# Kernel optimization log

Measured on AMD Instinct MI355X. Metric: run time of the kernel, lower is better.

## Reference

```python
import jax, jax.numpy as jnp
import numpy as np

B, C_ENC, H, W = 8, 512, 96, 96
N_SAMP = 64            # num_samples in forward
N_NODES = 2 * N_SAMP   # 64 pos + 64 neg per image
D = 256                # node feature dim after head_in_ln
N_HEADS = 8
DH = D // N_HEADS
SINKHORN_ITERS = 10


def _ln(x):
    # LayerNorm(elementwise_affine=False)
    m = x.mean(-1, keepdims=True)
    v = x.var(-1, keepdims=True)
    return (x - m) / jnp.sqrt(v + 1e-5)


def setup_inputs() -> dict:
    key = jax.random.key(0)
    ks = jax.random.split(key, 12)
    std = 0.01  # matches nn.init.normal_(std=0.01) in _init_weights
    inp = {
        "feat_s": jax.random.normal(ks[0], (B, C_ENC, H, W), jnp.float32),
        "score_s": jax.random.normal(ks[1], (B, 1, H, W), jnp.float32),
        "feat_t": jax.random.normal(ks[2], (B, C_ENC, H, W), jnp.float32),
        "score_t": jax.random.normal(ks[3], (B, 1, H, W), jnp.float32),
        "head_W1": std * jax.random.normal(ks[4], (C_ENC, D), jnp.float32),
        "head_b1": jnp.zeros((D,), jnp.float32),
        "head_W2": std * jax.random.normal(ks[5], (D, D), jnp.float32),
        "head_b2": jnp.zeros((D,), jnp.float32),
        "intra_W": jax.random.normal(ks[6], (4, D, D), jnp.float32) / jnp.sqrt(jnp.float32(D)),
        "intra_b": jnp.zeros((4, D), jnp.float32),
        "cross_W": jax.random.normal(ks[7], (4, D, D), jnp.float32) / jnp.sqrt(jnp.float32(D)),
        "cross_b": jnp.zeros((4, D), jnp.float32),
        "cls_W1": std * jax.random.normal(ks[8], (D, 128), jnp.float32),
        "cls_b1": jnp.zeros((128,), jnp.float32),
        "cls_W2": std * jax.random.normal(ks[9], (128, 1), jnp.float32),
        "cls_b2": jnp.zeros((1,), jnp.float32),
        "aff_A": jax.random.normal(ks[10], (D, D), jnp.float32) / jnp.sqrt(jnp.float32(D)),
    }
    return inp


def _sample_points(feat, score):
    # torch version: boolean-mask nonzero + random gather of 64 pos / 64 neg spatial
    # locations per image. JIT-friendly deterministic equivalent: top-64 highest
    # sigmoid scores = positives, top-64 lowest = negatives.
    s = jax.nn.sigmoid(score[:, 0].reshape(B, -1))            # [B, H*W]
    _, pos_idx = jax.lax.top_k(s, N_SAMP)
    _, neg_idx = jax.lax.top_k(-s, N_SAMP)
    idx = jnp.concatenate([pos_idx, neg_idx], axis=1)         # [B, 128]
    ff = feat.reshape(B, C_ENC, -1)                           # [B, 512, H*W]
    nodes = jnp.take_along_axis(ff, idx[:, None, :], axis=2)  # [B, 512, 128]
    nodes = nodes.transpose(0, 2, 1)                          # [B, 128, 512]
    labels = jnp.concatenate(
        [jnp.ones((B, N_SAMP, 1), feat.dtype), jnp.zeros((B, N_SAMP, 1), feat.dtype)], axis=1)
    return nodes, labels


def _mha(xq, xkv, Wp, bp):
    # standard multi-head attention (MultiHeadAttentionWrapper)
    q = xq @ Wp[0] + bp[0]
    k = xkv @ Wp[1] + bp[1]
    v = xkv @ Wp[2] + bp[2]
    sh = lambda t: t.reshape(t.shape[0], t.shape[1], N_HEADS, DH)
    att = jnp.einsum("bqhd,bkhd->bhqk", sh(q), sh(k)) / jnp.sqrt(jnp.float32(DH))
    att = jax.nn.softmax(att, axis=-1)
    o = jnp.einsum("bhqk,bkhd->bqhd", att, sh(v)).reshape(xq.shape[0], xq.shape[1], D)
    return o @ Wp[3] + bp[3], att.mean(1)


def _forward(feat_s, score_s, feat_t, score_t, head_W1, head_b1, head_W2, head_b2,
             intra_W, intra_b, cross_W, cross_b, cls_W1, cls_b1, cls_W2, cls_b2, aff_A):
    n1, l1 = _sample_points(feat_s, score_s)
    n2, l2 = _sample_points(feat_t, score_t)

    # head_in_ln: Linear -> LN -> ReLU -> Linear -> LN
    head = lambda x: _ln(jax.nn.relu(_ln(x @ head_W1 + head_b1)) @ head_W2 + head_b2)
    n1, n2 = head(n1), head(n2)

    # intra-domain graph (self-attention), shared weights for both domains
    n1, _ = _mha(n1, n1, intra_W, intra_b)
    n2, _ = _mha(n2, n2, intra_W, intra_b)

    # cross-domain graph (cross-attention both directions, shared weights)
    c1, _ = _mha(n1, n2, cross_W, cross_b)
    c2, _ = _mha(n2, n1, cross_W, cross_b)
    n1, n2 = c1, c2

    # node classification loss (BCEWithLogits, mean)
    cls = lambda x: jax.nn.relu(x @ cls_W1 + cls_b1) @ cls_W2 + cls_b2
    def bce_logits(logit, lab):
        return jnp.mean(jnp.maximum(logit, 0) - logit * lab + jnp.log1p(jnp.exp(-jnp.abs(logit))))
    node_loss = bce_logits(cls(n1), l1) + bce_logits(cls(n2), l2)

    # affinity + InstanceNorm2d(1) + sinkhorn refine
    Mmat = jnp.einsum("bnd,de,bme->bnm", n1, aff_A, n2)       # [B, 128, 128]
    mu = Mmat.mean((1, 2), keepdims=True)
    var = Mmat.var((1, 2), keepdims=True)
    K = (Mmat - mu) / jnp.sqrt(var + 1e-5)
    for _ in range(SINKHORN_ITERS):  # log-space row/col normalization
        K = K - jax.nn.logsumexp(K, axis=2, keepdims=True)
        K = K - jax.nn.logsumexp(K, axis=1, keepdims=True)
    P = jnp.exp(K)

    # matching loss = BCEFocalLoss(gamma=2, alpha=0.25) vs label-agreement matrix
    gt = (l1[:, :, 0][:, :, None] == l2[:, :, 0][:, None, :]).astype(P.dtype)
    pt = jnp.clip(P, 1e-6, 1.0 - 1e-6)
    mat_loss = jnp.mean(-0.25 * (1 - pt) ** 2 * gt * jnp.log(pt)
                        - 0.75 * pt ** 2 * (1 - gt) * jnp.log(1 - pt))

    total_loss = node_loss + 10.0 * mat_loss
    return n1, total_loss


def reference(feat_s, score_s, feat_t, score_t, head_W1, head_b1, head_W2, head_b2,
              intra_W, intra_b, cross_W, cross_b, cls_W1, cls_b1, cls_W2, cls_b2, aff_A):
    return _forward(feat_s, score_s, feat_t, score_t, head_W1, head_b1, head_W2, head_b2,
                    intra_W, intra_b, cross_W, cross_b, cls_W1, cls_b1, cls_W2, cls_b2, aff_A)
```

## Files before the change

### kernel.cpp

```cpp
#include <hip/hip_runtime.h>
#include <math.h>

#define BIMG 8
#define HW 9216
#define CENC 512
#define NN 128
#define DD 256
#define NHEAD 8
#define DH 32
#define ROWS1 1024
#define ROWS2 2048
#define TAILB 520

typedef unsigned long long ull;
typedef __attribute__((ext_vector_type(4))) float f32x4;
typedef __attribute__((ext_vector_type(4))) unsigned u32x4;
typedef __attribute__((ext_vector_type(2))) unsigned u32x2;

__device__ __forceinline__ unsigned short f2bf(float f) {
  unsigned u = __float_as_uint(f);
  u += 0x7fffu + ((u >> 16) & 1u);
  return (unsigned short)(u >> 16);
}
__device__ __forceinline__ float bf2f(unsigned h) { return __uint_as_float(h << 16); }
__device__ __forceinline__ unsigned pack2(float a, float b) {
  return (unsigned)f2bf(a) | ((unsigned)f2bf(b) << 16);
}

__device__ __forceinline__ ull cmpex_keep(ull k, ull o, bool keepMax) {
  return ((k > o) == keepMax) ? k : o;
}
__device__ __forceinline__ void bsort64(ull& k, int lane) {
#pragma unroll
  for (int size = 2; size <= 64; size <<= 1) {
#pragma unroll
    for (int stride = size >> 1; stride > 0; stride >>= 1) {
      ull o = __shfl_xor(k, stride);
      bool keepMax = (((lane & size) == 0) == ((lane & stride) == 0));
      k = cmpex_keep(k, o, keepMax);
    }
  }
}
__device__ __forceinline__ void bmerge64(ull& top, ull b, int lane) {
  ull rev = __shfl_xor(b, 63);
  ull m = top > rev ? top : rev;
#pragma unroll
  for (int stride = 32; stride > 0; stride >>= 1) {
    ull o = __shfl_xor(m, stride);
    m = cmpex_keep(m, o, (lane & stride) == 0);
  }
  top = m;
}

__global__ __launch_bounds__(256) void head_kernel(const float* __restrict__ score_s,
                                                   const float* __restrict__ score_t,
                                                   int* __restrict__ idx_out,
                                                   float* __restrict__ loss_acc,
                                                   const float* __restrict__ hw1,
                                                   const float* __restrict__ hw2,
                                                   const float* __restrict__ iw,
                                                   const float* __restrict__ cw,
                                                   const float* __restrict__ aw,
                                                   const float* __restrict__ clsW1,
                                                   unsigned short* __restrict__ wt,
                                                   unsigned short* __restrict__ w1t) {
  __shared__ ull sm[256];
  __shared__ float tile[32][33];
  int tid = threadIdx.x;
  if (blockIdx.x < 32) {
    int blk = blockIdx.x;
    int bi = blk >> 1, neg = blk & 1;
    int lane = tid & 63, w = tid >> 6;
    if (blk == 0 && tid < 4) loss_acc[tid] = 0.f;
    const float* sp = (bi < 8 ? score_s : score_t) + (size_t)(bi & 7) * HW;
    int q0 = w * 36;
    ull keys[36];
#pragma unroll
    for (int j = 0; j < 36; ++j) {
      float x = sp[(q0 + j) * 64 + lane];
      unsigned ub = __float_as_uint(x);
      unsigned u = (ub & 0x80000000u) ? ~ub : (ub | 0x80000000u);
      if (neg) u = ~u;
      int gi = (q0 + j) * 64 + lane;
      keys[j] = ((ull)u << 32) | (unsigned)(~gi);
    }
    ull top1 = keys[0];  bsort64(top1, lane);
    ull top2 = keys[18]; bsort64(top2, lane);
#pragma unroll
    for (int j = 1; j < 18; ++j) {
      ull k1 = keys[j], k2 = keys[18 + j];
      bsort64(k1, lane);
      bsort64(k2, lane);
      bmerge64(top1, k1, lane);
      bmerge64(top2, k2, lane);
    }
    bmerge64(top1, top2, lane);
    sm[w * 64 + lane] = top1;
    __syncthreads();
    if (w < 2) {
      ull a = sm[(2 * w) * 64 + lane];
      ull b = sm[(2 * w + 1) * 64 + (63 - lane)];
      ull m = a > b ? a : b;
#pragma unroll
      for (int stride = 32; stride > 0; stride >>= 1) {
        ull o = __shfl_xor(m, stride);
        m = cmpex_keep(m, o, (lane & stride) == 0);
      }
      sm[(2 * w) * 64 + lane] = m;
    }
    __syncthreads();
    if (w == 0) {
      ull a = sm[lane];
      ull b = sm[128 + (63 - lane)];
      ull m = a > b ? a : b;
#pragma unroll
      for (int stride = 32; stride > 0; stride >>= 1) {
        ull o = __shfl_xor(m, stride);
        m = cmpex_keep(m, o, (lane & stride) == 0);
      }
      idx_out[bi * NN + neg * 64 + lane] = (int)(~(unsigned)(m & 0xffffffffull));
    }
  } else if (blockIdx.x < 800) {
    int bid = blockIdx.x - 32;
    const float* src; unsigned short* dst; int K, k0, n0;
    if (bid < 128) {
      src = hw1; dst = wt; K = 512;
      k0 = (bid >> 3) * 32; n0 = (bid & 7) * 32;
    } else {
      int id2 = bid - 128;
      int m = id2 >> 6, tt = id2 & 63;
      K = 256;
      k0 = (tt >> 3) * 32; n0 = (tt & 7) * 32;
      src = (m == 0) ? hw2 : (m < 5) ? iw + (size_t)(m - 1) * 65536
          : (m < 9) ? cw + (size_t)(m - 5) * 65536 : aw;
      dst = wt + 131072 + (size_t)m * 65536;
    }
    int r = tid >> 3, c = (tid & 7) * 4;
    float4 v = *(const float4*)&src[(size_t)(k0 + r) * 256 + n0 + c];
    tile[r][c] = v.x; tile[r][c + 1] = v.y; tile[r][c + 2] = v.z; tile[r][c + 3] = v.w;
    __syncthreads();
    u32x2 o;
    o[0] = pack2(tile[c][r], tile[c + 1][r]);
    o[1] = pack2(tile[c + 2][r], tile[c + 3][r]);
    *(u32x2*)&dst[(size_t)(n0 + r) * K + k0 + c] = o;
  } else {
    int bid3 = blockIdx.x - 800;
    int k0 = (bid3 >> 2) * 32, n0 = (bid3 & 3) * 32;
    int r = tid >> 3, c = (tid & 7) * 4;
    float4 v = *(const float4*)&clsW1[(size_t)(k0 + r) * 128 + n0 + c];
    tile[r][c] = v.x; tile[r][c + 1] = v.y; tile[r][c + 2] = v.z; tile[r][c + 3] = v.w;
    __syncthreads();
    u32x2 o;
    o[0] = pack2(tile[c][r], tile[c + 1][r]);
    o[1] = pack2(tile[c + 2][r], tile[c + 3][r]);
    *(u32x2*)&w1t[(size_t)(n0 + r) * 256 + k0 + c] = o;
  }
}

__global__ __launch_bounds__(256) void gather_kernel(const float* __restrict__ feat_s,
                                                     const float* __restrict__ feat_t,
                                                     const int* __restrict__ idx,
                                                     unsigned short* __restrict__ nodes) {
  int blk = blockIdx.x;
  int bi = blk >> 7, n = blk & 127;
  int b = bi & 7;
  const float* fp = (bi < 8) ? feat_s : feat_t;
  int pos = idx[bi * NN + n];
  const float* src = fp + (size_t)b * CENC * HW + pos;
  unsigned* dst = (unsigned*)(nodes + (size_t)blk * CENC);
  int t = threadIdx.x;
  float f0 = src[(size_t)(2 * t) * HW];
  float f1 = src[(size_t)(2 * t + 1) * HW];
  dst[t] = pack2(f0, f1);
}

template<int K>
__global__ __launch_bounds__(256) void gemm_mf(const unsigned short* __restrict__ A,
                                               const unsigned short* __restrict__ Wt,
                                               const float* __restrict__ bias,
                                               unsigned short* __restrict__ Cb,
                                               float* __restrict__ Cf,
                                               int ldc, int f32rows,
                                               const float* __restrict__ in_stats, int in_relu,
                                               float* __restrict__ out_stats,
                                               int Az, int Wz, int Cbz, int Cfz, int bz) {
  constexpr int LDK = K + 8;
  constexpr int KC = K / 8;
  __shared__ unsigned short As[32][LDK];
  __shared__ unsigned short Bs[64][LDK];
  __shared__ float mS[32], rS[32];
  int z = blockIdx.z;
  A  += (size_t)z * Az;
  Wt += (size_t)z * Wz;
  if (Cb)   Cb += (size_t)z * Cbz;
  if (Cf)   Cf += (size_t)z * Cfz;
  if (bias) bias += (size_t)z * bz;
  int n0 = blockIdx.x * 64, m0 = blockIdx.y * 32;
  int t = threadIdx.x;
  if (in_stats) {
    if (t < 32) {
      const float* sp = in_stats + (size_t)(m0 + t) * 16;
      float s = 0.f, q = 0.f;
#pragma unroll
      for (int i = 0; i < 8; ++i) { s += sp[i]; q += sp[8 + i]; }
      float m = s * (1.0f / 256.f);
      float var = q * (1.0f / 256.f) - m * m;
      mS[t] = m;
      rS[t] = 1.0f / sqrtf(var + 1e-5f);
    }
    __syncthreads();
  }
  for (int i = t; i < 32 * KC; i += 256) {
    int row = i / KC, c8 = (i % KC) * 8;
    u32x4 av = *(const u32x4*)&A[(size_t)(m0 + row) * K + c8];
    if (in_stats) {
      float m = mS[row], r = rS[row];
#pragma unroll
      for (int j = 0; j < 4; ++j) {
        float f0 = (bf2f(av[j] & 0xffffu) - m) * r;
        float f1 = (bf2f(av[j] >> 16) - m) * r;
        if (in_relu) { f0 = fmaxf(f0, 0.f); f1 = fmaxf(f1, 0.f); }
        av[j] = pack2(f0, f1);
      }
    }
    *(u32x4*)&As[row][c8] = av;
  }
  for (int i = t; i < 64 * KC; i += 256) {
    int row = i / KC, c8 = (i % KC) * 8;
    *(u32x4*)&Bs[row][c8] = *(const u32x4*)&Wt[(size_t)(n0 + row) * K + c8];
  }
  __syncthreads();
  int l = t & 63, w = t >> 6;
  int wr = w >> 1, wc = w & 1;
  int fra = wr * 16 + (l & 15);
  int frk = (l >> 4) * 8;
  int fb0 = wc * 32 + (l & 15), fb1 = fb0 + 16;
  f32x4 acc0 = {0.f, 0.f, 0.f, 0.f};
  f32x4 acc1 = {0.f, 0.f, 0.f, 0.f};
#pragma unroll
  for (int ks = 0; ks < K / 32; ++ks) {
    u32x4 af = *(const u32x4*)&As[fra][ks * 32 + frk];
    u32x4 b0 = *(const u32x4*)&Bs[fb0][ks * 32 + frk];
    u32x4 b1 = *(const u32x4*)&Bs[fb1][ks * 32 + frk];
    asm volatile("v_mfma_f32_16x16x32_bf16 %0, %1, %2, %0" : "+v"(acc0) : "v"(af), "v"(b0));
    asm volatile("v_mfma_f32_16x16x32_bf16 %0, %1, %2, %0" : "+v"(acc1) : "v"(af), "v"(b1));
  }
  asm volatile("s_nop 7\n\ts_nop 7" ::);
  int col0 = n0 + wc * 32 + (l & 15);
  int rbase = m0 + wr * 16 + (l >> 4) * 4;
  float b0 = 0.f, b1 = 0.f;
  if (bias) { b0 = bias[col0]; b1 = bias[col0 + 16]; }
#pragma unroll
  for (int r = 0; r < 4; ++r) {
    int row = rbase + r;
    float o0 = acc0[r] + b0;
    float o1 = acc1[r] + b1;
    if (Cb) {
      Cb[(size_t)row * 256 + col0]      = f2bf(o0);
      Cb[(size_t)row * 256 + col0 + 16] = f2bf(o1);
    }
    if (Cf && row < f32rows) {
      Cf[(size_t)row * ldc + col0]      = o0;
      Cf[(size_t)row * ldc + col0 + 16] = o1;
    }
    if (out_stats) {
      float s = o0 + o1, q = o0 * o0 + o1 * o1;
#pragma unroll
      for (int m = 1; m < 16; m <<= 1) { s += __shfl_xor(s, m); q += __shfl_xor(q, m); }
      if ((l & 15) == 0) {
        out_stats[(size_t)row * 16 + blockIdx.x * 2 + wc]     = s;
        out_stats[(size_t)row * 16 + 8 + blockIdx.x * 2 + wc] = q;
      }
    }
  }
}

__global__ __launch_bounds__(256) void attn_kernel(const unsigned short* __restrict__ q,
                                                   const unsigned short* __restrict__ k,
                                                   const unsigned short* __restrict__ v,
                                                   unsigned short* __restrict__ o, int swap) {
  __shared__ __align__(16) float Ks[NN][DH];
  __shared__ __align__(16) float Vs[NN][DH];
  __shared__ __align__(16) float Ex[64][3][34];
  int blk = blockIdx.x;
  int bb = blk >> 4, h = (blk >> 1) & 7, qh = blk & 1;
  int kb = swap ? (bb ^ 8) : bb;
  int t = threadIdx.x;
  int rr = t & 63, part = t >> 6;
  for (int e = t; e < 1024; e += 256) {
    int which = e >> 9;
    int idx2 = e & 511;
    int r = idx2 >> 2, c8 = (idx2 & 3) * 8;
    u32x4 val = *(const u32x4*)&(which ? v : k)[(size_t)(kb * NN + r) * DD + h * DH + c8];
    float* dst = which ? &Vs[r][c8] : &Ks[r][c8];
#pragma unroll
    for (int i = 0; i < 4; ++i) {
      dst[2 * i]     = bf2f(val[i] & 0xffffu);
      dst[2 * i + 1] = bf2f(val[i] >> 16);
    }
  }
  __syncthreads();
  int qrow = bb * NN + qh * 64 + rr;
  float4 q4[8];
  {
    const unsigned short* qp = q + (size_t)qrow * DD + h * DH;
#pragma unroll
    for (int c4 = 0; c4 < 4; ++c4) {
      u32x4 u = *(const u32x4*)&qp[c4 * 8];
      q4[c4 * 2].x = bf2f(u[0] & 0xffffu); q4[c4 * 2].y = bf2f(u[0] >> 16);
      q4[c4 * 2].z = bf2f(u[1] & 0xffffu); q4[c4 * 2].w = bf2f(u[1] >> 16);
      q4[c4 * 2 + 1].x = bf2f(u[2] & 0xffffu); q4[c4 * 2 + 1].y = bf2f(u[2] >> 16);
      q4[c4 * 2 + 1].z = bf2f(u[3] & 0xffffu); q4[c4 * 2 + 1].w = bf2f(u[3] >> 16);
    }
  }
  const float scale = 0.17677669529663687f;
  int j0 = part * 32;
  float mx = -1e30f;
  for (int j = j0; j < j0 + 32; ++j) {
    const float4* kp = (const float4*)Ks[j];
    float s = 0.f;
#pragma unroll
    for (int c4 = 0; c4 < 8; ++c4) {
      float4 kv = kp[c4];
      s += q4[c4].x * kv.x + q4[c4].y * kv.y + q4[c4].z * kv.z + q4[c4].w * kv.w;
    }
    mx = fmaxf(mx, s * scale);
  }
  float acc[DH];
#pragma unroll
  for (int c = 0; c < DH; ++c) acc[c] = 0.f;
  float den = 0.f;
  for (int j = j0; j < j0 + 32; ++j) {
    const float4* kp = (const float4*)Ks[j];
    float s = 0.f;
#pragma unroll
    for (int c4 = 0; c4 < 8; ++c4) {
      float4 kv = kp[c4];
      s += q4[c4].x * kv.x + q4[c4].y * kv.y + q4[c4].z * kv.z + q4[c4].w * kv.w;
    }
    float e = __expf(s * scale - mx);
    den += e;
    const float4* vp = (const float4*)Vs[j];
#pragma unroll
    for (int c4 = 0; c4 < 8; ++c4) {
      float4 vv = vp[c4];
      acc[c4 * 4 + 0] += e * vv.x; acc[c4 * 4 + 1] += e * vv.y;
      acc[c4 * 4 + 2] += e * vv.z; acc[c4 * 4 + 3] += e * vv.w;
    }
  }
  if (part) {
#pragma unroll
    for (int c = 0; c < DH; ++c) Ex[rr][part - 1][c] = acc[c];
    Ex[rr][part - 1][32] = mx;
    Ex[rr][part - 1][33] = den;
  }
  __syncthreads();
  if (part == 0) {
    float M = mx;
#pragma unroll
    for (int p = 0; p < 3; ++p) M = fmaxf(M, Ex[rr][p][32]);
    float f0 = __expf(mx - M);
    float fp[3];
    float dt = den * f0;
#pragma unroll
    for (int p = 0; p < 3; ++p) { fp[p] = __expf(Ex[rr][p][32] - M); dt += Ex[rr][p][33] * fp[p]; }
    float inv = 1.0f / dt;
    unsigned ovu[16];
#pragma unroll
    for (int c = 0; c < 16; ++c) {
      float x0 = acc[2 * c] * f0, x1 = acc[2 * c + 1] * f0;
#pragma unroll
      for (int p = 0; p < 3; ++p) { x0 += Ex[rr][p][2 * c] * fp[p]; x1 += Ex[rr][p][2 * c + 1] * fp[p]; }
      ovu[c] = pack2(x0 * inv, x1 * inv);
    }
    unsigned* op = (unsigned*)(o + (size_t)qrow * DD + h * DH);
#pragma unroll
    for (int i = 0; i < 4; ++i) {
      u32x4 w4;
      w4[0] = ovu[4 * i]; w4[1] = ovu[4 * i + 1]; w4[2] = ovu[4 * i + 2]; w4[3] = ovu[4 * i + 3];
      *(u32x4*)&op[4 * i] = w4;
    }
  }
}

struct SkSmem {
  union { unsigned short tmpL[128][264]; float Km[128][132]; } u;
  float u_[NN];
  float v_[NN];
  float red[20];
};
struct ClsSmem {
  float xs[4][256];
  float part[4][128];
  float red[8];
};
union TailSmem { SkSmem sk; ClsSmem cls; };

__device__ __forceinline__ void ticket_finalize(float* acc, float* out) {
  __threadfence();
  int tk = atomicAdd((int*)acc + 3, 1);
  if (tk == TAILB - 1) {
    float a0 = atomicAdd(acc + 0, 0.0f);
    float a1 = atomicAdd(acc + 1, 0.0f);
    out[ROWS1 * DD] = a0 + 10.0f * a1;
  }
}

__global__ __launch_bounds__(1024) void tail_kernel(const unsigned short* __restrict__ bufH,
                                                    const unsigned short* __restrict__ wt_af,
                                                    const unsigned short* __restrict__ w1t,
                                                    const float* __restrict__ b1,
                                                    const float* __restrict__ W2,
                                                    const float* __restrict__ b2,
                                                    float* __restrict__ acc,
                                                    float* __restrict__ out) {
  __shared__ TailSmem sm;
  int t = threadIdx.x;
  int bid = blockIdx.x;
  if (bid < 8) {
    int b = bid;
    int l = t & 63, w = t >> 6;
    int tr = w >> 1;
    const unsigned short* c1 = bufH + (size_t)(b * 128) * 256;
    const unsigned short* c2 = bufH + (size_t)(1024 + b * 128) * 256;
    {
      int tcB = (w & 1) * 8;
      f32x4 accA[8];
#pragma unroll
      for (int i = 0; i < 8; ++i) accA[i] = (f32x4){0.f, 0.f, 0.f, 0.f};
      for (int ks = 0; ks < 8; ++ks) {
        int kk = ks * 32 + (l >> 4) * 8;
        u32x4 af = *(const u32x4*)&c1[(size_t)(tr * 16 + (l & 15)) * 256 + kk];
#pragma unroll
        for (int i = 0; i < 8; ++i) {
          u32x4 bf = *(const u32x4*)&wt_af[(size_t)((tcB + i) * 16 + (l & 15)) * 256 + kk];
          asm volatile("v_mfma_f32_16x16x32_bf16 %0, %1, %2, %0" : "+v"(accA[i]) : "v"(af), "v"(bf));
        }
      }
      asm volatile("s_nop 7\n\ts_nop 7" ::);
      int rb = tr * 16 + (l >> 4) * 4;
#pragma unroll
      for (int i = 0; i < 8; ++i) {
        int col = (tcB + i) * 16 + (l & 15);
#pragma unroll
        for (int r = 0; r < 4; ++r)
          sm.sk.u.tmpL[rb + r][col] = f2bf(accA[i][r]);
      }
    }
    __syncthreads();
    f32x4 accB[4];
    {
      int tcB = (w & 1) * 4;
#pragma unroll
      for (int i = 0; i < 4; ++i) accB[i] = (f32x4){0.f, 0.f, 0.f, 0.f};
      for (int ks = 0; ks < 8; ++ks) {
        int kk = ks * 32 + (l >> 4) * 8;
        u32x4 af = *(const u32x4*)&sm.sk.u.tmpL[tr * 16 + (l & 15)][kk];
#pragma unroll
        for (int i = 0; i < 4; ++i) {
          u32x4 bf = *(const u32x4*)&c2[(size_t)((tcB + i) * 16 + (l & 15)) * 256 + kk];
          asm volatile("v_mfma_f32_16x16x32_bf16 %0, %1, %2, %0" : "+v"(accB[i]) : "v"(af), "v"(bf));
        }
      }
      asm volatile("s_nop 7\n\ts_nop 7" ::);
    }
    __syncthreads();
    {
      int tcB = (w & 1) * 4;
      int rb = tr * 16 + (l >> 4) * 4;
#pragma unroll
      for (int i = 0; i < 4; ++i) {
        int col = (tcB + i) * 16 + (l & 15);
#pragma unroll
        for (int r = 0; r < 4; ++r)
          sm.sk.u.Km[rb + r][col] = accB[i][r];
      }
    }
    __syncthreads();
    int r = t >> 3, cg = t & 7;
    int c = t >> 3, rg = t & 7;
    float kr[16], kc[16];
    {
#pragma unroll
      for (int q4 = 0; q4 < 4; ++q4) {
        float4 f = *(const float4*)&sm.sk.u.Km[r][cg * 16 + q4 * 4];
        kr[q4 * 4 + 0] = f.x; kr[q4 * 4 + 1] = f.y; kr[q4 * 4 + 2] = f.z; kr[q4 * 4 + 3] = f.w;
      }
#pragma unroll
      for (int q = 0; q < 16; ++q)
        kc[q] = sm.sk.u.Km[rg * 16 + q][c];
    }
    float s = 0.f;
#pragma unroll
    for (int q = 0; q < 16; ++q) s += kr[q];
    for (int m = 1; m < 64; m <<= 1) s += __shfl_xor(s, m);
    if ((t & 63) == 0) sm.sk.red[t >> 6] = s;
    __syncthreads();
    if (t == 0) { float tt = 0.f; for (int i = 0; i < 16; ++i) tt += sm.sk.red[i]; sm.sk.red[16] = tt; }
    __syncthreads();
    float mu = sm.sk.red[16] * (1.0f / 16384.f);
    __syncthreads();
    float sq = 0.f;
#pragma unroll
    for (int q = 0; q < 16; ++q) { float d = kr[q] - mu; sq += d * d; }
    for (int m = 1; m < 64; m <<= 1) sq += __shfl_xor(sq, m);
    if ((t & 63) == 0) sm.sk.red[t >> 6] = sq;
    __syncthreads();
    if (t == 0) { float tt = 0.f; for (int i = 0; i < 16; ++i) tt += sm.sk.red[i]; sm.sk.red[17] = tt; }
    __syncthreads();
    float inv = 1.0f / sqrtf(sm.sk.red[17] * (1.0f / 16384.f) + 1e-5f);
#pragma unroll
    for (int q = 0; q < 16; ++q) { kr[q] = (kr[q] - mu) * inv; kc[q] = (kc[q] - mu) * inv; }
    if (t < NN) { sm.sk.u_[t] = 0.f; sm.sk.v_[t] = 0.f; }
    __syncthreads();
    for (int iter = 0; iter < 10; ++iter) {
      float tmp[16];
      {
        const float4* vp = (const float4*)(sm.sk.v_ + cg * 16);
#pragma unroll
        for (int q4 = 0; q4 < 4; ++q4) {
          float4 f = vp[q4];
          tmp[q4 * 4 + 0] = kr[q4 * 4 + 0] - f.x; tmp[q4 * 4 + 1] = kr[q4 * 4 + 1] - f.y;
          tmp[q4 * 4 + 2] = kr[q4 * 4 + 2] - f.z; tmp[q4 * 4 + 3] = kr[q4 * 4 + 3] - f.w;
        }
        float mx = tmp[0];
#pragma unroll
        for (int q = 1; q < 16; ++q) mx = fmaxf(mx, tmp[q]);
        for (int m = 1; m < 8; m <<= 1) mx = fmaxf(mx, __shfl_xor(mx, m));
        float smv = 0.f;
#pragma unroll
        for (int q = 0; q < 16; ++q) smv += __expf(tmp[q] - mx);
        for (int m = 1; m < 8; m <<= 1) smv += __shfl_xor(smv, m);
        if (cg == 0) sm.sk.u_[r] = mx + __logf(smv);
      }
      __syncthreads();
      {
        const float4* up = (const float4*)(sm.sk.u_ + rg * 16);
#pragma unroll
        for (int q4 = 0; q4 < 4; ++q4) {
          float4 f = up[q4];
          tmp[q4 * 4 + 0] = kc[q4 * 4 + 0] - f.x; tmp[q4 * 4 + 1] = kc[q4 * 4 + 1] - f.y;
          tmp[q4 * 4 + 2] = kc[q4 * 4 + 2] - f.z; tmp[q4 * 4 + 3] = kc[q4 * 4 + 3] - f.w;
        }
        float mx = tmp[0];
#pragma unroll
        for (int q = 1; q < 16; ++q) mx = fmaxf(mx, tmp[q]);
        for (int m = 1; m < 8; m <<= 1) mx = fmaxf(mx, __shfl_xor(mx, m));
        float smv = 0.f;
#pragma unroll
        for (int q = 0; q < 16; ++q) smv += __expf(tmp[q] - mx);
        for (int m = 1; m < 8; m <<= 1) smv += __shfl_xor(smv, m);
        if (rg == 0) sm.sk.v_[c] = mx + __logf(smv);
      }
      __syncthreads();
    }
    float ur = sm.sk.u_[r];
    float fsum = 0.f;
    {
      const float4* vp = (const float4*)(sm.sk.v_ + cg * 16);
#pragma unroll
      for (int q4 = 0; q4 < 4; ++q4) {
        float4 f = vp[q4];
        float vv[4] = {f.x, f.y, f.z, f.w};
#pragma unroll
        for (int j = 0; j < 4; ++j) {
          float P = __expf(kr[q4 * 4 + j] - ur - vv[j]);
          float pt = fminf(fmaxf(P, 1e-6f), 1.0f - 1e-6f);
          int col = cg * 16 + q4 * 4 + j;
          bool gt = (r < 64) == (col < 64);
          float wgt = gt ? (-0.25f * (1.f - pt) * (1.f - pt)) : (-0.75f * pt * pt);
          float lg = gt ? __logf(pt) : __logf(1.f - pt);
          fsum += wgt * lg;
        }
      }
    }
    for (int m = 1; m < 64; m <<= 1) fsum += __shfl_xor(fsum, m);
    if ((t & 63) == 0) sm.sk.red[t >> 6] = fsum;
    __syncthreads();
    if (t == 0) {
      float tt = 0.f; for (int i = 0; i < 16; ++i) tt += sm.sk.red[i];
      atomicAdd(acc + 1, tt * (1.0f / 131072.f));
      ticket_finalize(acc, out);
    }
  } else {
    int row0 = (bid - 8) * 4;
    {
      int rr = t >> 8, cc = t & 255;
      sm.cls.xs[rr][cc] = bf2f(bufH[(size_t)(row0 + rr) * 256 + cc]);
    }
    __syncthreads();
    int grp = t >> 8, col = t & 127, kh = (t >> 7) & 1;
    const unsigned short* wp = w1t + (size_t)col * 256 + kh * 128;
    const float* xp = &sm.cls.xs[grp][kh * 128];
    float h = 0.f;
#pragma unroll
    for (int i = 0; i < 16; ++i) {
      u32x4 wv = *(const u32x4*)&wp[i * 8];
      const float* x8 = xp + i * 8;
      h += x8[0] * bf2f(wv[0] & 0xffffu) + x8[1] * bf2f(wv[0] >> 16)
         + x8[2] * bf2f(wv[1] & 0xffffu) + x8[3] * bf2f(wv[1] >> 16)
         + x8[4] * bf2f(wv[2] & 0xffffu) + x8[5] * bf2f(wv[2] >> 16)
         + x8[6] * bf2f(wv[3] & 0xffffu) + x8[7] * bf2f(wv[3] >> 16);
    }
    if (kh == 1) sm.cls.part[grp][col] = h;
    __syncthreads();
    if (kh == 0) {
      float z = h + sm.cls.part[grp][col] + b1[col];
      float p = fmaxf(z, 0.f) * W2[col];
#pragma unroll
      for (int m = 1; m < 64; m <<= 1) p += __shfl_xor(p, m);
      if ((t & 63) == 0) sm.cls.red[grp * 2 + ((t >> 6) & 1)] = p;
    }
    __syncthreads();
    if (t == 0) {
      float total = 0.f;
      float bb2 = b2[0];
#pragma unroll
      for (int g = 0; g < 4; ++g) {
        float z = sm.cls.red[2 * g] + sm.cls.red[2 * g + 1] + bb2;
        float lab = (((row0 + g) & 127) < 64) ? 1.f : 0.f;
        total += fmaxf(z, 0.f) - z * lab + log1pf(__expf(-fabsf(z)));
      }
      atomicAdd(acc, total * (1.0f / 1024.0f));
      ticket_finalize(acc, out);
    }
  }
}

extern "C" void kernel_launch(void* const* d_in, const int* in_sizes, int n_in,
                              void* d_out, int out_size, void* d_ws, size_t ws_size,
                              hipStream_t stream) {
  const float* feat_s  = (const float*)d_in[0];
  const float* score_s = (const float*)d_in[1];
  const float* feat_t  = (const float*)d_in[2];
  const float* score_t = (const float*)d_in[3];
  const float* head_W1 = (const float*)d_in[4];
  const float* head_b1 = (const float*)d_in[5];
  const float* head_W2 = (const float*)d_in[6];
  const float* head_b2 = (const float*)d_in[7];
  const float* intra_W = (const float*)d_in[8];
  const float* intra_b = (const float*)d_in[9];
  const float* cross_W = (const float*)d_in[10];
  const float* cross_b = (const float*)d_in[11];
  const float* cls_W1  = (const float*)d_in[12];
  const float* cls_b1  = (const float*)d_in[13];
  const float* cls_W2  = (const float*)d_in[14];
  const float* cls_b2  = (const float*)d_in[15];
  const float* aff_A   = (const float*)d_in[16];

  unsigned short* nodes_bf = (unsigned short*)d_ws;
  unsigned short* bufA_bf  = nodes_bf + 2048 * 512;
  unsigned short* bufB_bf  = bufA_bf + ROWS2 * DD;
  unsigned short* bufH_bf  = bufB_bf + ROWS2 * DD;
  unsigned short* qkv_bf   = bufH_bf + ROWS2 * DD;
  unsigned short* attn_bf  = qkv_bf + 3 * ROWS2 * DD;
  unsigned short* wt       = attn_bf + ROWS2 * DD;
  unsigned short* w1t      = wt + 786432;
  float* st1  = (float*)(w1t + 32768);
  float* st2  = st1 + ROWS2 * 16;
  float* acc  = st2 + ROWS2 * 16;
  int*   idxb = (int*)(acc + 8);
  float* out_f = (float*)d_out;

  unsigned short* wt_h1 = wt;
  unsigned short* wt_h2 = wt + 131072;
  unsigned short* wt_in = wt_h2 + 65536;
  unsigned short* wt_cr = wt_in + 4 * 65536;
  unsigned short* wt_af = wt_cr + 4 * 65536;

  head_kernel<<<832, 256, 0, stream>>>(score_s, score_t, idxb, acc,
                                       head_W1, head_W2, intra_W, cross_W, aff_A, cls_W1,
                                       wt, w1t);
  gather_kernel<<<2048, 256, 0, stream>>>(feat_s, feat_t, idxb, nodes_bf);

  dim3 g1(4, 64, 1);
  dim3 gq(4, 64, 3);
  const float* nulf = nullptr;
  float* nulw = nullptr;

  gemm_mf<512><<<g1, 256, 0, stream>>>(nodes_bf, wt_h1, head_b1, bufA_bf, nulw,
                                       0, 0, nulf, 0, st1, 0, 0, 0, 0, 0);
  gemm_mf<256><<<g1, 256, 0, stream>>>(bufA_bf, wt_h2, head_b2, bufB_bf, nulw,
                                       0, 0, st1, 1, st2, 0, 0, 0, 0, 0);
  gemm_mf<256><<<gq, 256, 0, stream>>>(bufB_bf, wt_in, intra_b, qkv_bf, nulw,
                                       0, 0, st2, 0, nulw, 0, 65536, ROWS2 * DD, 0, 256);
  attn_kernel<<<256, 256, 0, stream>>>(qkv_bf, qkv_bf + ROWS2 * DD, qkv_bf + 2 * ROWS2 * DD,
                                       attn_bf, 0);
  gemm_mf<256><<<g1, 256, 0, stream>>>(attn_bf, wt_in + 3 * 65536, intra_b + 768, bufH_bf, nulw,
                                       0, 0, nulf, 0, nulw, 0, 0, 0, 0, 0);
  gemm_mf<256><<<gq, 256, 0, stream>>>(bufH_bf, wt_cr, cross_b, qkv_bf, nulw,
                                       0, 0, nulf, 0, nulw, 0, 65536, ROWS2 * DD, 0, 256);
  attn_kernel<<<256, 256, 0, stream>>>(qkv_bf, qkv_bf + ROWS2 * DD, qkv_bf + 2 * ROWS2 * DD,
                                       attn_bf, 1);
  gemm_mf<256><<<g1, 256, 0, stream>>>(attn_bf, wt_cr + 3 * 65536, cross_b + 768, bufH_bf, out_f,
                                       256, ROWS1, nulf, 0, nulw, 0, 0, 0, 0, 0);
  tail_kernel<<<TAILB, 1024, 0, stream>>>(bufH_bf, wt_af, w1t, cls_b1, cls_W2, cls_b2,
                                          acc, out_f);
}
```

Baseline: 217.7 us.

## Fuse feature gather into first head GEMM and widen row statistics layout

Removes the separate gather kernel and the nodes buffer. A new gemm1_fused kernel gathers the 16 sampled feature rows per block straight into shared memory as bf16, runs the 512-wide head GEMM with MFMA, and writes bias-added outputs plus per-16-column partial sums for LayerNorm. The stats layout changes from 16 to 32 partials per row, and gemm_mf is updated to match. The goal is to avoid a global round trip and a launch, but the fused kernel only runs 128 blocks and reloads the full weight tile for each block.

Measured after the change: 216.8 us. No clear change (-0.4%).

```diff
diff --git a/kernel.cpp b/kernel.cpp
--- a/kernel.cpp
+++ b/kernel.cpp
@@ -13,18 +13,22 @@
 #define TAILB 520
 
 typedef unsigned long long ull;
+typedef unsigned short u16;
 typedef __attribute__((ext_vector_type(4))) float f32x4;
 typedef __attribute__((ext_vector_type(4))) unsigned u32x4;
 typedef __attribute__((ext_vector_type(2))) unsigned u32x2;
 
-__device__ __forceinline__ unsigned short f2bf(float f) {
+__device__ __forceinline__ u16 f2bf(float f) {
   unsigned u = __float_as_uint(f);
   u += 0x7fffu + ((u >> 16) & 1u);
-  return (unsigned short)(u >> 16);
+  return (u16)(u >> 16);
 }
 __device__ __forceinline__ float bf2f(unsigned h) { return __uint_as_float(h << 16); }
 __device__ __forceinline__ unsigned pack2(float a, float b) {
   return (unsigned)f2bf(a) | ((unsigned)f2bf(b) << 16);
+}
+__device__ __forceinline__ void mfma_b(f32x4& acc, u32x4 a, u32x4 b) {
+  asm volatile("v_mfma_f32_16x16x32_bf16 %0, %1, %2, %0" : "+v"(acc) : "v"(a), "v"(b));
 }
 
 __device__ __forceinline__ ull cmpex_keep(ull k, ull o, bool keepMax) {
@@ -62,8 +66,8 @@
                                                    const float* __restrict__ cw,
                                                    const float* __restrict__ aw,
                                                    const float* __restrict__ clsW1,
-                                                   unsigned short* __restrict__ wt,
-                                                   unsigned short* __restrict__ w1t) {
+                                                   u16* __restrict__ wt,
+                                                   u16* __restrict__ w1t) {
   __shared__ ull sm[256];
   __shared__ float tile[32][33];
   int tid = threadIdx.x;
@@ -122,7 +126,7 @@
     }
   } else if (blockIdx.x < 800) {
     int bid = blockIdx.x - 32;
-    const float* src; unsigned short* dst; int K, k0, n0;
+    const float* src; u16* dst; int K, k0, n0;
     if (bid < 128) {
       src = hw1; dst = wt; K = 512;
       k0 = (bid >> 3) * 32; n0 = (bid & 7) * 32;
@@ -157,28 +161,75 @@
   }
 }
 
-__global__ __launch_bounds__(256) void gather_kernel(const float* __restrict__ feat_s,
-                                                     const float* __restrict__ feat_t,
-                                                     const int* __restrict__ idx,
-                                                     unsigned short* __restrict__ nodes) {
-  int blk = blockIdx.x;
-  int bi = blk >> 7, n = blk & 127;
-  int b = bi & 7;
-  const float* fp = (bi < 8) ? feat_s : feat_t;
-  int pos = idx[bi * NN + n];
-  const float* src = fp + (size_t)b * CENC * HW + pos;
-  unsigned* dst = (unsigned*)(nodes + (size_t)blk * CENC);
-  int t = threadIdx.x;
-  float f0 = src[(size_t)(2 * t) * HW];
-  float f1 = src[(size_t)(2 * t + 1) * HW];
-  dst[t] = pack2(f0, f1);
+__global__ __launch_bounds__(256) void gemm1_fused(const float* __restrict__ feat_s,
+                                                   const float* __restrict__ feat_t,
+                                                   const int* __restrict__ idxb,
+                                                   const u16* __restrict__ wt_h1,
+                                                   const float* __restrict__ head_b1,
+                                                   u16* __restrict__ bufA,
+                                                   float* __restrict__ st1) {
+  __shared__ u16 As[16][520];
+  __shared__ u16 Bs[256][40];
+  int t = threadIdx.x, l = t & 63, cg = t >> 6;
+  int m0 = blockIdx.x * 16;
+#pragma unroll
+  for (int row = 0; row < 16; ++row) {
+    int grow = m0 + row;
+    int bi = grow >> 7, n = grow & 127, b = bi & 7;
+    const float* fp = (bi < 8) ? feat_s : feat_t;
+    int pos = idxb[bi * NN + n];
+    const float* src = fp + (size_t)b * CENC * HW + pos;
+    float f0 = src[(size_t)(2 * t) * HW];
+    float f1 = src[(size_t)(2 * t + 1) * HW];
+    *(unsigned*)&As[row][2 * t] = pack2(f0, f1);
+  }
+  __syncthreads();
+  f32x4 acc[4];
+#pragma unroll
+  for (int i = 0; i < 4; ++i) acc[i] = (f32x4){0.f, 0.f, 0.f, 0.f};
+  for (int kc = 0; kc < 16; ++kc) {
+#pragma unroll
+    for (int i = 0; i < 4; ++i) {
+      int e = t + i * 256;
+      int nn2 = e >> 2, ch8 = (e & 3) * 8;
+      *(u32x4*)&Bs[nn2][ch8] = *(const u32x4*)&wt_h1[(size_t)nn2 * 512 + kc * 32 + ch8];
+    }
+    __syncthreads();
+    u32x4 af = *(const u32x4*)&As[l & 15][kc * 32 + (l >> 4) * 8];
+#pragma unroll
+    for (int i = 0; i < 4; ++i) {
+      u32x4 bf = *(const u32x4*)&Bs[cg * 64 + i * 16 + (l & 15)][(l >> 4) * 8];
+      mfma_b(acc[i], af, bf);
+    }
+    __syncthreads();
+  }
+  asm volatile("s_nop 7\n\ts_nop 7" ::);
+  int rbase = m0 + (l >> 4) * 4;
+#pragma unroll
+  for (int i = 0; i < 4; ++i) {
+    int col = cg * 64 + i * 16 + (l & 15);
+    float bb = head_b1[col];
+#pragma unroll
+    for (int r = 0; r < 4; ++r) {
+      int row = rbase + r;
+      float o = acc[i][r] + bb;
+      bufA[(size_t)row * 256 + col] = f2bf(o);
+      float s = o, q = o * o;
+#pragma unroll
+      for (int m = 1; m < 16; m <<= 1) { s += __shfl_xor(s, m); q += __shfl_xor(q, m); }
+      if ((l & 15) == 0) {
+        st1[(size_t)row * 32 + cg * 4 + i]      = s;
+        st1[(size_t)row * 32 + 16 + cg * 4 + i] = q;
+      }
+    }
+  }
 }
 
 template<int K>
-__global__ __launch_bounds__(256) void gemm_mf(const unsigned short* __restrict__ A,
-                                               const unsigned short* __restrict__ Wt,
+__global__ __launch_bounds__(256) void gemm_mf(const u16* __restrict__ A,
+                                               const u16* __restrict__ Wt,
                                                const float* __restrict__ bias,
-                                               unsigned short* __restrict__ Cb,
+                                               u16* __restrict__ Cb,
                                                float* __restrict__ Cf,
                                                int ldc, int f32rows,
                                                const float* __restrict__ in_stats, int in_relu,
@@ -186,8 +237,8 @@
                                                int Az, int Wz, int Cbz, int Cfz, int bz) {
   constexpr int LDK = K + 8;
   constexpr int KC = K / 8;
-  __shared__ unsigned short As[32][LDK];
-  __shared__ unsigned short Bs[64][LDK];
+  __shared__ u16 As[32][LDK];
+  __shared__ u16 Bs[64][LDK];
   __shared__ float mS[32], rS[32];
   int z = blockIdx.z;
   A  += (size_t)z * Az;
@@ -199,14 +250,14 @@
   int t = threadIdx.x;
   if (in_stats) {
     if (t < 32) {
-      const float* sp = in_stats + (size_t)(m0 + t) * 16;
+      const float* sp = in_stats + (size_t)(m0 + t) * 32;
       float s = 0.f, q = 0.f;
 #pragma unroll
-      for (int i = 0; i < 8; ++i) { s += sp[i]; q += sp[8 + i]; }
-      float m = s * (1.0f / 256.f);
-      float var = q * (1.0f / 256.f) - m * m;
-      mS[t] = m;
-      rS[t] = 1.0f / sqrtf(var + 1e-5f);
+      for (int i = 0; i < 16; ++i) { s += sp[i]; q += sp[16 + i]; }
+      float mm = s * (1.f / 256.f);
+      float var = q * (1.f / 256.f) - mm * mm;
+      mS[t] = mm;
+      rS[t] = rsqrtf(fmaxf(var, 0.f) + 1e-5f);
     }
     __syncthreads();
   }
@@ -214,11 +265,11 @@
     int row = i / KC, c8 = (i % KC) * 8;
     u32x4 av = *(const u32x4*)&A[(size_t)(m0 + row) * K + c8];
     if (in_stats) {
-      float m = mS[row], r = rS[row];
+      float mm = mS[row], rr = rS[row];
 #pragma unroll
       for (int j = 0; j < 4; ++j) {
-        float f0 = (bf2f(av[j] & 0xffffu) - m) * r;
-        float f1 = (bf2f(av[j] >> 16) - m) * r;
+        float f0 = (bf2f(av[j] & 0xffffu) - mm) * rr;
+        float f1 = (bf2f(av[j] >> 16) - mm) * rr;
         if (in_relu) { f0 = fmaxf(f0, 0.f); f1 = fmaxf(f1, 0.f); }
         av[j] = pack2(f0, f1);
       }
@@ -242,8 +293,8 @@
     u32x4 af = *(const u32x4*)&As[fra][ks * 32 + frk];
     u32x4 b0 = *(const u32x4*)&Bs[fb0][ks * 32 + frk];
     u32x4 b1 = *(const u32x4*)&Bs[fb1][ks * 32 + frk];
-    asm volatile("v_mfma_f32_16x16x32_bf16 %0, %1, %2, %0" : "+v"(acc0) : "v"(af), "v"(b0));
-    asm volatile("v_mfma_f32_16x16x32_bf16 %0, %1, %2, %0" : "+v"(acc1) : "v"(af), "v"(b1));
+    mfma_b(acc0, af, b0);
+    mfma_b(acc1, af, b1);
   }
   asm volatile("s_nop 7\n\ts_nop 7" ::);
   int col0 = n0 + wc * 32 + (l & 15);
@@ -259,26 +310,32 @@
       Cb[(size_t)row * 256 + col0]      = f2bf(o0);
       Cb[(size_t)row * 256 + col0 + 16] = f2bf(o1);
     }
-    if (Cf && row < f32rows) {
+    if (Cf && row < ROWS1) {
       Cf[(size_t)row * ldc + col0]      = o0;
       Cf[(size_t)row * ldc + col0 + 16] = o1;
     }
     if (out_stats) {
-      float s = o0 + o1, q = o0 * o0 + o1 * o1;
-#pragma unroll
-      for (int m = 1; m < 16; m <<= 1) { s += __shfl_xor(s, m); q += __shfl_xor(q, m); }
+      float s0 = o0, q0 = o0 * o0, s1 = o1, q1 = o1 * o1;
+#pragma unroll
+      for (int m = 1; m < 16; m <<= 1) {
+        s0 += __shfl_xor(s0, m); q0 += __shfl_xor(q0, m);
+        s1 += __shfl_xor(s1, m); q1 += __shfl_xor(q1, m);
+      }
       if ((l & 15) == 0) {
-        out_stats[(size_t)row * 16 + blockIdx.x * 2 + wc]     = s;
-        out_stats[(size_t)row * 16 + 8 + blockIdx.x * 2 + wc] = q;
-      }
-    }
-  }
-}
-
-__global__ __launch_bounds__(256) void attn_kernel(const unsigned short* __restrict__ q,
-                                                   const unsigned short* __restrict__ k,
-                                                   const unsigned short* __restrict__ v,
-                                                   unsigned short* __restrict__ o, int swap) {
+        int base = (n0 >> 4) + wc * 2;
+        out_stats[(size_t)row * 32 + base]          = s0;
+        out_stats[(size_t)row * 32 + base + 1]      = s1;
+        out_stats[(size_t)row * 32 + 16 + base]     = q0;
+        out_stats[(size_t)row * 32 + 16 + base + 1] = q1;
+      }
+    }
+  }
+}
+
+__global__ __launch_bounds__(256) void attn_kernel(const u16* __restrict__ q,
+                                                   const u16* __restrict__ k,
+                                                   const u16* __restrict__ v,
+                                                   u16* __restrict__ o, int swap) {
   __shared__ __align__(16) float Ks[NN][DH];
   __shared__ __align__(16) float Vs[NN][DH];
   __shared__ __align__(16) float Ex[64][3][34];
@@ -303,7 +360,7 @@
   int qrow = bb * NN + qh * 64 + rr;
   float4 q4[8];
   {
-    const unsigned short* qp = q + (size_t)qrow * DD + h * DH;
+    const u16* qp = q + (size_t)qrow * DD + h * DH;
 #pragma unroll
     for (int c4 = 0; c4 < 4; ++c4) {
       u32x4 u = *(const u32x4*)&qp[c4 * 8];
@@ -384,7 +441,7 @@
 }
 
 struct SkSmem {
-  union { unsigned short tmpL[128][264]; float Km[128][132]; } u;
+  union { u16 tmpL[128][264]; float Km[128][133]; } u;
   float u_[NN];
   float v_[NN];
   float red[20];
@@ -406,9 +463,9 @@
   }
 }
 
-__global__ __launch_bounds__(1024) void tail_kernel(const unsigned short* __restrict__ bufH,
-                                                    const unsigned short* __restrict__ wt_af,
-                                                    const unsigned short* __restrict__ w1t,
+__global__ __launch_bounds__(1024) void tail_kernel(const u16* __restrict__ bufH,
+                                                    const u16* __restrict__ wt_af,
+                                                    const u16* __restrict__ w1t,
                                                     const float* __restrict__ b1,
                                                     const float* __restrict__ W2,
                                                     const float* __restrict__ b2,
@@ -421,8 +478,8 @@
     int b = bid;
     int l = t & 63, w = t >> 6;
     int tr = w >> 1;
-    const unsigned short* c1 = bufH + (size_t)(b * 128) * 256;
-    const unsigned short* c2 = bufH + (size_t)(1024 + b * 128) * 256;
+    const u16* c1 = bufH + (size_t)(b * 128) * 256;
+    const u16* c2 = bufH + (size_t)(1024 + b * 128) * 256;
     {
       int tcB = (w & 1) * 8;
       f32x4 accA[8];
@@ -434,7 +491,7 @@
 #pragma unroll
         for (int i = 0; i < 8; ++i) {
           u32x4 bf = *(const u32x4*)&wt_af[(size_t)((tcB + i) * 16 + (l & 15)) * 256 + kk];
-          asm volatile("v_mfma_f32_16x16x32_bf16 %0, %1, %2, %0" : "+v"(accA[i]) : "v"(af), "v"(bf));
+          mfma_b(accA[i], af, bf);
         }
       }
       asm volatile("s_nop 7\n\ts_nop 7" ::);
@@ -443,23 +500,23 @@
       for (int i = 0; i < 8; ++i) {
         int col = (tcB + i) * 16 + (l & 15);
 #pragma unroll
-        for (int r = 0; r < 4; ++r)
-          sm.sk.u.tmpL[rb + r][col] = f2bf(accA[i][r]);
-      }
-    }
-    __syncthreads();
-    f32x4 accB[4];
+        for (int r2 = 0; r2 < 4; ++r2)
+          sm.sk.u.tmpL[rb + r2][col] = f2bf(accA[i][r2]);
+      }
+    }
+    __syncthreads();
+    f32x4 aB[4];
     {
       int tcB = (w & 1) * 4;
 #pragma unroll
-      for (int i = 0; i < 4; ++i) accB[i] = (f32x4){0.f, 0.f, 0.f, 0.f};
+      for (int i = 0; i < 4; ++i) aB[i] = (f32x4){0.f, 0.f, 0.f, 0.f};
       for (int ks = 0; ks < 8; ++ks) {
         int kk = ks * 32 + (l >> 4) * 8;
         u32x4 af = *(const u32x4*)&sm.sk.u.tmpL[tr * 16 + (l & 15)][kk];
 #pragma unroll
         for (int i = 0; i < 4; ++i) {
           u32x4 bf = *(const u32x4*)&c2[(size_t)((tcB + i) * 16 + (l & 15)) * 256 + kk];
-          asm volatile("v_mfma_f32_16x16x32_bf16 %0, %1, %2, %0" : "+v"(accB[i]) : "v"(af), "v"(bf));
+          mfma_b(aB[i], af, bf);
         }
       }
       asm volatile("s_nop 7\n\ts_nop 7" ::);
@@ -472,8 +529,8 @@
       for (int i = 0; i < 4; ++i) {
         int col = (tcB + i) * 16 + (l & 15);
 #pragma unroll
-        for (int r = 0; r < 4; ++r)
-          sm.sk.u.Km[rb + r][col] = accB[i][r];
+        for (int r2 = 0; r2 < 4; ++r2)
+          sm.sk.u.Km[rb + r2][col] = aB[i][r2];
       }
     }
     __syncthreads();
@@ -590,7 +647,7 @@
     }
     __syncthreads();
     int grp = t >> 8, col = t & 127, kh = (t >> 7) & 1;
-    const unsigned short* wp = w1t + (size_t)col * 256 + kh * 128;
+    const u16* wp = w1t + (size_t)col * 256 + kh * 128;
     const float* xp = &sm.cls.xs[grp][kh * 128];
     float h = 0.f;
 #pragma unroll
@@ -648,52 +705,49 @@
   const float* cls_b2  = (const float*)d_in[15];
   const float* aff_A   = (const float*)d_in[16];
 
-  unsigned short* nodes_bf = (unsigned short*)d_ws;
-  unsigned short* bufA_bf  = nodes_bf + 2048 * 512;
-  unsigned short* bufB_bf  = bufA_bf + ROWS2 * DD;
-  unsigned short* bufH_bf  = bufB_bf + ROWS2 * DD;
-  unsigned short* qkv_bf   = bufH_bf + ROWS2 * DD;
-  unsigned short* attn_bf  = qkv_bf + 3 * ROWS2 * DD;
-  unsigned short* wt       = attn_bf + ROWS2 * DD;
-  unsigned short* w1t      = wt + 786432;
-  float* st1  = (float*)(w1t + 32768);
-  float* st2  = st1 + ROWS2 * 16;
-  float* acc  = st2 + ROWS2 * 16;
-  int*   idxb = (int*)(acc + 8);
+  u16* bufA  = (u16*)d_ws;
+  u16* bufB  = bufA + ROWS2 * DD;
+  u16* bufH  = bufB + ROWS2 * DD;
+  u16* qkv   = bufH + ROWS2 * DD;
+  u16* attnb = qkv + 3 * ROWS2 * DD;
+  u16* wt    = attnb + ROWS2 * DD;
+  u16* w1t   = wt + 786432;
+  float* st1 = (float*)(w1t + 32768);
+  float* st2 = st1 + ROWS2 * 32;
+  float* acc = st2 + ROWS2 * 32;
+  int* idxb  = (int*)(acc + 8);
   float* out_f = (float*)d_out;
 
-  unsigned short* wt_h1 = wt;
-  unsigned short* wt_h2 = wt + 131072;
-  unsigned short* wt_in = wt_h2 + 65536;
-  unsigned short* wt_cr = wt_in + 4 * 65536;
-  unsigned short* wt_af = wt_cr + 4 * 65536;
+  u16* wt_h1 = wt;
+  u16* wt_h2 = wt + 131072;
+  u16* wt_in = wt_h2 + 65536;
+  u16* wt_cr = wt_in + 4 * 65536;
+  u16* wt_af = wt_cr + 4 * 65536;
 
   head_kernel<<<832, 256, 0, stream>>>(score_s, score_t, idxb, acc,
                                        head_W1, head_W2, intra_W, cross_W, aff_A, cls_W1,
                                        wt, w1t);
-  gather_kernel<<<2048, 256, 0, stream>>>(feat_s, feat_t, idxb, nodes_bf);
+  gemm1_fused<<<128, 256, 0, stream>>>(feat_s, feat_t, idxb, wt_h1, head_b1, bufA, st1);
 
   dim3 g1(4, 64, 1);
   dim3 gq(4, 64, 3);
   const float* nulf = nullptr;
   float* nulw = nullptr;
 
-  gemm_mf<512><<<g1, 256, 0, stream>>>(nodes_bf, wt_h1, head_b1, bufA_bf, nulw,
-                                       0, 0, nulf, 0, st1, 0, 0, 0, 0, 0);
-  gemm_mf<256><<<g1, 256, 0, stream>>>(bufA_bf, wt_h2, head_b2, bufB_bf, nulw,
+  gemm_mf<256><<<g1, 256, 0, stream>>>(bufA, wt_h2, head_b2, bufB, nulw,
                                        0, 0, st1, 1, st2, 0, 0, 0, 0, 0);
-  gemm_mf<256><<<gq, 256, 0, stream>>>(bufB_bf, wt_in, intra_b, qkv_bf, nulw,
+  gemm_mf<256><<<gq, 256, 0, stream>>>(bufB, wt_in, intra_b, qkv, nulw,
                                        0, 0, st2, 0, nulw, 0, 65536, ROWS2 * DD, 0, 256);
-  attn_kernel<<<256, 256, 0, stream>>>(qkv_bf, qkv_bf + ROWS2 * DD, qkv_bf + 2 * ROWS2 * DD,
-                                       attn_bf, 0);
-  gemm_mf<256><<<g1, 256, 0, stream>>>(attn_bf, wt_in + 3 * 65536, intra_b + 768, bufH_bf, nulw,
+  attn_kernel<<<256, 256, 0, stream>>>(qkv, qkv + ROWS2 * DD, qkv + 2 * ROWS2 * DD,
+                                       attnb, 0);
+  gemm_mf<256><<<g1, 256, 0, stream>>>(attnb, wt_in + 3 * 65536, intra_b + 768, bufH, nulw,
                                        0, 0, nulf, 0, nulw, 0, 0, 0, 0, 0);
-  gemm_mf<256><<<gq, 256, 0, stream>>>(bufH_bf, wt_cr, cross_b, qkv_bf, nulw,
+  gemm_mf<256><<<gq, 256, 0, stream>>>(bufH, wt_cr, cross_b, qkv, nulw,
                                        0, 0, nulf, 0, nulw, 0, 65536, ROWS2 * DD, 0, 256);
-  attn_kernel<<<256, 256, 0, stream>>>(qkv_bf, qkv_bf + ROWS2 * DD, qkv_bf + 2 * ROWS2 * DD,
-                                       attn_bf, 1);
-  gemm_mf<256><<<g1, 256, 0, stream>>>(attn_bf, wt_cr + 3 * 65536, cross_b + 768, bufH_bf, out_f,
-                                       256, ROWS1, nulf, 0, nulw, 0, 0, 0, 0, 0);
-  tail_kernel<<<TAILB, 1024, 0, stream>>>(bufH_bf, wt_af, w1t, cls_b1, cls_W2, cls_b2,
+  attn_kernel<<<256, 256, 0, stream>>>(qkv, qkv + ROWS2 * DD, qkv + 2 * ROWS2 * DD,
+                                       attnb, 1);
+  gemm_mf<256><<<g1, 256, 0, stream>>>(attnb, wt_cr + 3 * 65536, cross_b + 768, bufH, out_f,
+                                       256, 0, nulf, 0, nulw, 0, 0, 0, 0, 0);
+  tail_kernel<<<TAILB, 1024, 0, stream>>>(bufH, wt_af, w1t, cls_b1, cls_W2, cls_b2,
                                           acc, out_f);
 }
```
